# Optimization experiments

Hardware: AMD Instinct MI355X
Metric: run time of the kernel (lower is better)

The kernel has to match this reference:

```python
import jax, jax.numpy as jnp
import numpy as np

B = 128        # graphs
N_PER = 1024   # nodes per graph
K = 7          # knn neighbors
X_SIZE = 16
POS_SIZE = 3
H1, H2 = 64, 128
N = B * N_PER
EPS = 1e-5


def _lin_init(key, din, dout):
    kw, kb = jax.random.split(key)
    s = 1.0 / np.sqrt(din)
    w = jax.random.uniform(kw, (din, dout), jnp.float32, -s, s)
    b = jax.random.uniform(kb, (dout,), jnp.float32, -s, s)
    return w, b


def setup_inputs() -> dict:
    key = jax.random.key(0)
    ks = jax.random.split(key, 12)
    x = jax.random.normal(ks[0], (N, X_SIZE), jnp.float32)
    pos = jax.random.normal(ks[1], (N, POS_SIZE), jnp.float32)
    batch = jnp.repeat(jnp.arange(B, dtype=jnp.int32), N_PER)
    wk1, bk1 = _lin_init(ks[2], X_SIZE, H1)
    wq1, bq1 = _lin_init(ks[3], X_SIZE, H1)
    wv1, bv1 = _lin_init(ks[4], X_SIZE, H1)
    ws1, bs1 = _lin_init(ks[5], X_SIZE, H1)
    wk2, bk2 = _lin_init(ks[6], H1, H2)
    wq2, bq2 = _lin_init(ks[7], H1, H2)
    wv2, bv2 = _lin_init(ks[8], H1, H2)
    ws2, bs2 = _lin_init(ks[9], H1, H2)
    g1 = jnp.ones((H1,), jnp.float32); be1 = jnp.zeros((H1,), jnp.float32)
    g2 = jnp.ones((H2,), jnp.float32); be2 = jnp.zeros((H2,), jnp.float32)
    return dict(x=x, pos=pos, batch=batch,
                wk1=wk1, bk1=bk1, wq1=wq1, bq1=bq1, wv1=wv1, bv1=bv1, ws1=ws1, bs1=bs1, g1=g1, be1=be1,
                wk2=wk2, bk2=bk2, wq2=wq2, bq2=bq2, wv2=wv2, bv2=bv2, ws2=ws2, bs2=bs2, g2=g2, be2=be2)


def knn_edges(pos):
    # batch-aware kNN: graphs are equal-sized contiguous blocks of N_PER nodes
    p = pos.reshape(B, N_PER, POS_SIZE)
    def per_graph(pg):
        d = jnp.sum((pg[:, None, :] - pg[None, :, :]) ** 2, axis=-1)  # [n, n]
        d = jnp.where(jnp.eye(N_PER, dtype=bool), jnp.inf, d)          # no self loops
        _, idx = jax.lax.top_k(-d, K)                                   # [n, K]
        return idx
    idx = jax.vmap(per_graph)(p)                       # [B, N_PER, K]
    offs = (jnp.arange(B) * N_PER)[:, None, None]
    src = (idx + offs).reshape(-1)                     # neighbor j (source)
    dst = jnp.broadcast_to(jnp.arange(N_PER)[None, :, None] + offs, (B, N_PER, K)).reshape(-1)
    return src, dst


def res_gated_conv(x, src, dst, wk, bk, wq, bq, wv, bv, ws, bs):
    # out_i = skip(x_i) + sum_{j->i} sigmoid(K x_i + Q x_j) * V x_j
    kf = x @ wk + bk
    qf = x @ wq + bq
    vf = x @ wv + bv
    msg = jax.nn.sigmoid(kf[dst] + qf[src]) * vf[src]  # [E, out]
    agg = jnp.zeros_like(kf).at[dst].add(msg)
    return agg + x @ ws + bs


def batch_norm(x, gamma, beta):
    m = x.mean(0)
    v = jnp.mean((x - m) ** 2, 0)  # biased var (training-mode BN)
    return (x - m) * jax.lax.rsqrt(v + EPS) * gamma + beta


def reference(x, pos, batch, wk1, bk1, wq1, bq1, wv1, bv1, ws1, bs1, g1, be1,
              wk2, bk2, wq2, bq2, wv2, bv2, ws2, bs2, g2, be2):
    src, dst = knn_edges(pos)
    h = jax.nn.relu(batch_norm(res_gated_conv(x, src, dst, wk1, bk1, wq1, bq1, wv1, bv1, ws1, bs1), g1, be1))
    h = jax.nn.relu(batch_norm(res_gated_conv(h, src, dst, wk2, bk2, wq2, bq2, wv2, bv2, ws2, bs2), g2, be2))
    s = jax.ops.segment_sum(h, batch, num_segments=B)
    cnt = jax.ops.segment_sum(jnp.ones((h.shape[0], 1), h.dtype), batch, num_segments=B)
    return s / cnt
```

## Files before the change

kernel.cpp:

```cpp
#include <hip/hip_runtime.h>
#include <hip/hip_bf16.h>

#define BGR   128
#define NPER  1024
#define NK    7
#define NNODES (BGR*NPER)

typedef __attribute__((ext_vector_type(8))) short short8;
typedef __attribute__((ext_vector_type(8))) unsigned short ushort8;
typedef __attribute__((ext_vector_type(4))) float floatx4;

static __device__ __forceinline__ float bf2f(unsigned short u) {
    unsigned int x = ((unsigned int)u) << 16;
    return __builtin_bit_cast(float, x);
}
static __device__ __forceinline__ unsigned short f2bf(float f) {
    unsigned int x = __builtin_bit_cast(unsigned int, f);
    unsigned int lsb = (x >> 16) & 1u;
    x += 0x7fffu + lsb;
    return (unsigned short)(x >> 16);
}

__global__ __launch_bounds__(256) void knn_kernel(const float* __restrict__ pos,
                                                  int* __restrict__ idx) {
    __shared__ __align__(16) floatx4 sp[NPER];
    __shared__ float ex[256][9];
    int g     = blockIdx.x >> 3;
    int qbase = (blockIdx.x & 7) << 7;
    int base  = g * NPER;
    const float* pg = pos + (size_t)base * 3;
    for (int t = threadIdx.x; t < NPER * 3; t += 256) {
        float v = pg[t];
        int j = t / 3, comp = t - j * 3;
        ((float*)&sp[j])[comp] = v;
    }
    __syncthreads();
    for (int j = threadIdx.x; j < NPER; j += 256) {
        floatx4 q = sp[j];
        sp[j].w = fmaf(q.x, q.x, fmaf(q.y, q.y, q.z * q.z));
    }
    __syncthreads();

    int qi = qbase + (threadIdx.x & 127);
    int hf = threadIdx.x >> 7;
    floatx4 me = sp[qi];
    float m2x = -2.f * me.x, m2y = -2.f * me.y, m2z = -2.f * me.z;

    float b0=3e38f,b1=3e38f,b2=3e38f,b3=3e38f,b4=3e38f,b5=3e38f,b6=3e38f,b7=3e38f;
    int j0base = hf << 9;
    for (int j0 = j0base; j0 < j0base + 512; j0 += 8) {
        #pragma unroll
        for (int u = 0; u < 8; ++u) {
            floatx4 q = sp[j0 + u];
            float d = fmaf(m2x, q.x, fmaf(m2y, q.y, fmaf(m2z, q.z, q.w)));
            unsigned int ub = (__builtin_bit_cast(unsigned int, d) & 0xFFFFFC00u)
                              | (unsigned int)(j0 + u);
            float t = __builtin_bit_cast(float, ub);
            float n7 = __builtin_amdgcn_fmed3f(b6, b7, t);
            float n6 = __builtin_amdgcn_fmed3f(b5, b6, t);
            float n5 = __builtin_amdgcn_fmed3f(b4, b5, t);
            float n4 = __builtin_amdgcn_fmed3f(b3, b4, t);
            float n3 = __builtin_amdgcn_fmed3f(b2, b3, t);
            float n2 = __builtin_amdgcn_fmed3f(b1, b2, t);
            float n1 = __builtin_amdgcn_fmed3f(b0, b1, t);
            b0 = fminf(b0, t);
            b1 = n1; b2 = n2; b3 = n3; b4 = n4; b5 = n5; b6 = n6; b7 = n7;
        }
    }
    float* er = ex[threadIdx.x];
    er[0]=b0; er[1]=b1; er[2]=b2; er[3]=b3; er[4]=b4; er[5]=b5; er[6]=b6; er[7]=b7;
    __syncthreads();
    if (threadIdx.x < 128) {
        int sh = qi >> 9;
        const float* A  = ex[threadIdx.x + (sh << 7)];
        const float* Bo = ex[threadIdx.x + ((1 - sh) << 7)];
        int* op = idx + (size_t)(base + qi) * NK;
        #pragma unroll
        for (int i = 0; i < 7; ++i) {
            float mm = fminf(A[i + 1], Bo[6 - i]);
            op[i] = base + (int)(__builtin_bit_cast(unsigned int, mm) & 1023u);
        }
    }
}

__global__ __launch_bounds__(256) void feat1_kernel(
    const float* __restrict__ x,
    const float* __restrict__ wk, const float* __restrict__ bk,
    const float* __restrict__ wq, const float* __restrict__ bq,
    const float* __restrict__ wv, const float* __restrict__ bv,
    const float* __restrict__ wsm, const float* __restrict__ bs,
    unsigned int* __restrict__ qv, unsigned int* __restrict__ ks) {
    int c = threadIdx.x & 63;
    float Wk[16], Wq[16], Wv[16], Ws[16];
    #pragma unroll
    for (int k = 0; k < 16; ++k) {
        Wk[k] = wk[k*64+c]; Wq[k] = wq[k*64+c]; Wv[k] = wv[k*64+c]; Ws[k] = wsm[k*64+c];
    }
    float Bk = bk[c], Bq = bq[c], Bv = bv[c], Bs = bs[c];
    int wave = blockIdx.x * (blockDim.x >> 6) + (threadIdx.x >> 6);
    int nw   = gridDim.x * (blockDim.x >> 6);
    for (int n = wave; n < NNODES; n += nw) {
        const float* xr = x + (size_t)n * 16;
        float ak = Bk, aq = Bq, av = Bv, as = Bs;
        #pragma unroll
        for (int k = 0; k < 16; ++k) {
            float xv = xr[k];
            ak += xv * Wk[k]; aq += xv * Wq[k]; av += xv * Wv[k]; as += xv * Ws[k];
        }
        size_t o = (size_t)n * 64 + c;
        qv[o] = ((unsigned int)f2bf(av) << 16) | f2bf(aq);
        ks[o] = ((unsigned int)f2bf(as) << 16) | f2bf(ak);
    }
}

template<int C>
__global__ __launch_bounds__(256) void conv_kernel(
    const unsigned int* __restrict__ qv, const unsigned int* __restrict__ ks,
    const int* __restrict__ idx, unsigned short* __restrict__ h,
    float* __restrict__ part) {
    const int NPB = 256 / C;
    int c   = threadIdx.x & (C - 1);
    int sub = __builtin_amdgcn_readfirstlane((int)(threadIdx.x / C));
    int b     = blockIdx.x;
    int xcd   = b & 7;
    int chunk = b >> 3;
    int graph = xcd * 16 + (chunk >> 5);
    int nblk  = chunk & 31;
    int n0 = graph * NPER + nblk * 32;
    float s = 0.f, s2 = 0.f;
    #pragma unroll 2
    for (int i = sub; i < 32; i += NPB) {
        int n = n0 + i;
        const int* nb = idx + (size_t)n * NK;
        unsigned int ku = ks[(size_t)n * C + c];
        float kv  = bf2f((unsigned short)(ku & 0xFFFF));
        float acc = bf2f((unsigned short)(ku >> 16));
        #pragma unroll
        for (int k = 0; k < NK; ++k) {
            int j = __builtin_amdgcn_readfirstlane(nb[k]);
            const unsigned int* p = qv + (size_t)j * C;
            unsigned int u = p[c];
            float qvv = bf2f((unsigned short)(u & 0xFFFF));
            float vvv = bf2f((unsigned short)(u >> 16));
            float t = kv + qvv;
            float sg = __builtin_amdgcn_rcpf(1.f + __expf(-t));
            acc = fmaf(sg, vvv, acc);
        }
        unsigned short hb = f2bf(acc);
        h[(size_t)n * C + c] = hb;
        float hv = bf2f(hb);
        s += hv; s2 += hv * hv;
    }
    __shared__ float ls[256], ls2[256];
    ls[threadIdx.x] = s; ls2[threadIdx.x] = s2;
    __syncthreads();
    if (threadIdx.x < C) {
        #pragma unroll
        for (int l = 1; l < NPB; ++l) { s += ls[threadIdx.x + l*C]; s2 += ls2[threadIdx.x + l*C]; }
        part[(size_t)blockIdx.x * 2 * C + threadIdx.x]     = s;
        part[(size_t)blockIdx.x * 2 * C + C + threadIdx.x] = s2;
    }
}

template<int C>
static __device__ __forceinline__ void bnfin_body(
    const float* __restrict__ part, const float* __restrict__ gamma,
    const float* __restrict__ beta, float* __restrict__ ss,
    int c, float* ls, float* ls2) {
    float s = 0.f, s2 = 0.f;
    for (int b = threadIdx.x; b < 4096; b += 256) {
        s  += part[(size_t)b * 2 * C + c];
        s2 += part[(size_t)b * 2 * C + C + c];
    }
    ls[threadIdx.x] = s; ls2[threadIdx.x] = s2;
    __syncthreads();
    for (int st = 128; st > 0; st >>= 1) {
        if (threadIdx.x < st) { ls[threadIdx.x] += ls[threadIdx.x+st]; ls2[threadIdx.x] += ls2[threadIdx.x+st]; }
        __syncthreads();
    }
    if (threadIdx.x == 0) {
        float m   = ls[0] / (float)NNODES;
        float var = ls2[0] / (float)NNODES - m * m;
        float inv = rsqrtf(var + 1e-5f);
        float sc  = gamma[c] * inv;
        ss[c]     = sc;
        ss[C + c] = beta[c] - m * sc;
    }
}

template<int C>
__global__ __launch_bounds__(256) void bnfin_kernel(
    const float* __restrict__ part, const float* __restrict__ gamma,
    const float* __restrict__ beta, float* __restrict__ ss) {
    __shared__ float ls[256], ls2[256];
    bnfin_body<C>(part, gamma, beta, ss, blockIdx.x, ls, ls2);
}

__global__ __launch_bounds__(256) void fin1_wfrag_kernel(
    const float* __restrict__ part, const float* __restrict__ gamma,
    const float* __restrict__ beta, float* __restrict__ ss,
    const float* __restrict__ w0, const float* __restrict__ w1,
    const float* __restrict__ w2, const float* __restrict__ w3,
    unsigned short* __restrict__ frag) {
    __shared__ float ls[256], ls2[256];
    if (blockIdx.x < 64) {
        bnfin_body<64>(part, gamma, beta, ss, blockIdx.x, ls, ls2);
        return;
    }
    int s  = blockIdx.x - 64;
    if (threadIdx.x >= 64) return;
    int m  = s >> 4;
    int kt = (s >> 3) & 1;
    int ct = s & 7;
    const float* w = (m == 0) ? w0 : (m == 1) ? w1 : (m == 2) ? w2 : w3;
    int l = threadIdx.x;
    int col = ct * 16 + (l & 15);
    int kbase = kt * 32 + (l >> 4) * 8;
    unsigned short* out = frag + ((size_t)s * 64 + l) * 8;
    #pragma unroll
    for (int e = 0; e < 8; ++e) out[e] = f2bf(w[(size_t)(kbase + e) * 128 + col]);
}

__global__ __launch_bounds__(256) void feat2_kernel(
    const unsigned short* __restrict__ h1n, const unsigned short* __restrict__ frag,
    const float* __restrict__ ss1,
    const float* __restrict__ b0, const float* __restrict__ b1,
    const float* __restrict__ b2, const float* __restrict__ b3,
    unsigned int* __restrict__ qv2, unsigned int* __restrict__ ks2) {
    __shared__ unsigned short xh[2][2][16][17];
    int nt = blockIdx.x;
    int m  = threadIdx.x >> 6;
    int l  = threadIdx.x & 63;
    const float* bm = (m == 0) ? b0 : (m == 1) ? b1 : (m == 2) ? b2 : b3;
    int lr = l & 15;
    int gq = l >> 4;
    int n  = nt * 16 + lr;
    const unsigned short* ar = h1n + (size_t)n * 64 + gq * 8;
    short8 a0r = *(const short8*)ar;
    short8 a1r = *(const short8*)(ar + 32);
    short8 a0, a1;
    #pragma unroll
    for (int e = 0; e < 8; ++e) {
        int c0 = gq * 8 + e;
        float f0 = bf2f((unsigned short)a0r[e]) * ss1[c0] + ss1[64 + c0];
        a0[e] = (short)f2bf(fmaxf(f0, 0.f));
        int c1 = 32 + gq * 8 + e;
        float f1 = bf2f((unsigned short)a1r[e]) * ss1[c1] + ss1[64 + c1];
        a1[e] = (short)f2bf(fmaxf(f1, 0.f));
    }
    #pragma unroll
    for (int ct = 0; ct < 8; ++ct) {
        size_t fb0 = ((size_t)(m * 16 + ct)     * 64 + l) * 8;
        size_t fb1 = ((size_t)(m * 16 + 8 + ct) * 64 + l) * 8;
        short8 w0 = *(const short8*)(frag + fb0);
        short8 w1 = *(const short8*)(frag + fb1);
        float bv = bm[ct * 16 + lr];
        floatx4 acc = {bv, bv, bv, bv};
        acc = __builtin_amdgcn_mfma_f32_16x16x32_bf16(a0, w0, acc, 0, 0, 0);
        acc = __builtin_amdgcn_mfma_f32_16x16x32_bf16(a1, w1, acc, 0, 0, 0);
        if (m >= 2) {
            #pragma unroll
            for (int r = 0; r < 4; ++r)
                xh[ct & 1][m - 2][gq * 4 + r][lr] = f2bf(acc[r]);
        }
        __syncthreads();
        if (m < 2) {
            unsigned int* od = (m == 1) ? qv2 : ks2;
            int set = (m == 1) ? 0 : 1;
            #pragma unroll
            for (int r = 0; r < 4; ++r) {
                unsigned int lo = f2bf(acc[r]);
                unsigned int hi = xh[ct & 1][set][gq * 4 + r][lr];
                od[(size_t)(nt * 16 + gq * 4 + r) * 128 + ct * 16 + lr] = (hi << 16) | lo;
            }
        }
    }
}

__global__ __launch_bounds__(256) void pool_partial_kernel(const unsigned short* __restrict__ h2,
                                                           const float* __restrict__ ss2,
                                                           float* __restrict__ part) {
    int g = blockIdx.x >> 2;
    int q = blockIdx.x & 3;
    int c = threadIdx.x & 127;
    int isub = threadIdx.x >> 7;
    float sc = ss2[c], sh = ss2[128 + c];
    float acc = 0.f;
    const unsigned short* hp = h2 + ((size_t)g * NPER + q * 256) * 128;
    for (int i = isub; i < 256; i += 2)
        acc += fmaxf(bf2f(hp[(size_t)i * 128 + c]) * sc + sh, 0.f);
    __shared__ float red[256];
    red[threadIdx.x] = acc;
    __syncthreads();
    if (threadIdx.x < 128)
        part[(size_t)blockIdx.x * 128 + c] = acc + red[threadIdx.x + 128];
}

__global__ void pool_final_kernel(const float* __restrict__ part, float* __restrict__ out) {
    int g = blockIdx.x, c = threadIdx.x;
    float s = part[(size_t)(g*4+0)*128+c] + part[(size_t)(g*4+1)*128+c]
            + part[(size_t)(g*4+2)*128+c] + part[(size_t)(g*4+3)*128+c];
    out[(size_t)g * 128 + c] = s * (1.f / 1024.f);
}

extern "C" void kernel_launch(void* const* d_in, const int* in_sizes, int n_in,
                              void* d_out, int out_size, void* d_ws, size_t ws_size,
                              hipStream_t stream) {
    const float* x   = (const float*)d_in[0];
    const float* pos = (const float*)d_in[1];
    const float* wk1 = (const float*)d_in[3];
    const float* bk1 = (const float*)d_in[4];
    const float* wq1 = (const float*)d_in[5];
    const float* bq1 = (const float*)d_in[6];
    const float* wv1 = (const float*)d_in[7];
    const float* bv1 = (const float*)d_in[8];
    const float* ws1 = (const float*)d_in[9];
    const float* bs1 = (const float*)d_in[10];
    const float* g1  = (const float*)d_in[11];
    const float* be1 = (const float*)d_in[12];
    const float* wk2 = (const float*)d_in[13];
    const float* bk2 = (const float*)d_in[14];
    const float* wq2 = (const float*)d_in[15];
    const float* bq2 = (const float*)d_in[16];
    const float* wv2 = (const float*)d_in[17];
    const float* bv2 = (const float*)d_in[18];
    const float* ws2 = (const float*)d_in[19];
    const float* bs2 = (const float*)d_in[20];
    const float* g2  = (const float*)d_in[21];
    const float* be2 = (const float*)d_in[22];
    float* out = (float*)d_out;

    const size_t SZ_QV1 = (size_t)NNODES * 64 * 4;
    const size_t SZ_QV2 = (size_t)NNODES * 128 * 4;

    char* ws = (char*)d_ws;
    size_t off = 0;
    auto alloc = [&](size_t b) { size_t o = off; off += (b + 255) & ~(size_t)255; return o; };

    int* idx              = (int*)(ws + alloc((size_t)NNODES * NK * 4));
    size_t o_region       = alloc(2 * SZ_QV2);
    unsigned int* qv1     = (unsigned int*)(ws + o_region);
    unsigned int* ks1     = (unsigned int*)(ws + o_region + SZ_QV1);
    unsigned int* qv2     = (unsigned int*)(ws + o_region);
    unsigned int* ks2     = (unsigned int*)(ws + o_region + SZ_QV2);
    unsigned short* h1    = (unsigned short*)(ws + alloc((size_t)NNODES * 64 * 2));
    unsigned short* h2    = (unsigned short*)(ws + alloc((size_t)NNODES * 128 * 2));
    unsigned short* frag  = (unsigned short*)(ws + alloc(64 * 64 * 8 * 2));
    float* part           = (float*)(ws + alloc((size_t)4096 * 2 * 128 * 4));
    float* ss1            = (float*)(ws + alloc(2 * 64 * 4));
    float* ss2            = (float*)(ws + alloc(2 * 128 * 4));
    (void)ws_size; (void)in_sizes; (void)n_in; (void)out_size;

    knn_kernel<<<BGR * 8, 256, 0, stream>>>(pos, idx);
    feat1_kernel<<<1024, 256, 0, stream>>>(x, wk1, bk1, wq1, bq1, wv1, bv1, ws1, bs1,
                                           qv1, ks1);
    conv_kernel<64><<<NNODES / 32, 256, 0, stream>>>(qv1, ks1, idx, h1, part);
    fin1_wfrag_kernel<<<128, 256, 0, stream>>>(part, g1, be1, ss1,
                                               wk2, wq2, wv2, ws2, frag);
    feat2_kernel<<<NNODES / 16, 256, 0, stream>>>(h1, frag, ss1, bk2, bq2, bv2, bs2,
                                                  qv2, ks2);
    conv_kernel<128><<<NNODES / 32, 256, 0, stream>>>(qv2, ks2, idx, h2, part);
    bnfin_kernel<128><<<128, 256, 0, stream>>>(part, g2, be2, ss2);
    pool_partial_kernel<<<BGR * 4, 256, 0, stream>>>(h2, ss2, part);
    pool_final_kernel<<<BGR, 128, 0, stream>>>(part, out);
}
```

Baseline: 257.3 us.

## Precompute padded positions globally and read kNN candidates via uniform scalar loads

Adds a small prep kernel that writes each position as a float4 with its squared norm in the w lane. The kNN kernel drops its shared-memory staging and two barriers and instead loads candidate points straight from global memory. Because the half index is made wave-uniform with readfirstlane, those loads can become scalar loads. This removes LDS traffic and the sync overhead from the inner loop, at the cost of one extra kernel launch and relying on scalar-cache hits.

```diff
diff --git a/kernel.cpp b/kernel.cpp
--- a/kernel.cpp
+++ b/kernel.cpp
@@ -21,37 +21,39 @@
     return (unsigned short)(x >> 16);
 }
 
-__global__ __launch_bounds__(256) void knn_kernel(const float* __restrict__ pos,
+__global__ __launch_bounds__(256) void prep_pos_kernel(const float* __restrict__ pos,
+                                                       floatx4* __restrict__ p4) {
+    int i = blockIdx.x * 256 + threadIdx.x;
+    if (i < NNODES) {
+        float x = pos[(size_t)i*3], y = pos[(size_t)i*3+1], z = pos[(size_t)i*3+2];
+        floatx4 v;
+        v.x = x; v.y = y; v.z = z;
+        v.w = fmaf(x, x, fmaf(y, y, z * z));
+        p4[i] = v;
+    }
+}
+
+__global__ __launch_bounds__(256) void knn_kernel(const floatx4* __restrict__ p4,
                                                   int* __restrict__ idx) {
-    __shared__ __align__(16) floatx4 sp[NPER];
     __shared__ float ex[256][9];
     int g     = blockIdx.x >> 3;
     int qbase = (blockIdx.x & 7) << 7;
     int base  = g * NPER;
-    const float* pg = pos + (size_t)base * 3;
-    for (int t = threadIdx.x; t < NPER * 3; t += 256) {
-        float v = pg[t];
-        int j = t / 3, comp = t - j * 3;
-        ((float*)&sp[j])[comp] = v;
-    }
-    __syncthreads();
-    for (int j = threadIdx.x; j < NPER; j += 256) {
-        floatx4 q = sp[j];
-        sp[j].w = fmaf(q.x, q.x, fmaf(q.y, q.y, q.z * q.z));
-    }
-    __syncthreads();
-
     int qi = qbase + (threadIdx.x & 127);
-    int hf = threadIdx.x >> 7;
-    floatx4 me = sp[qi];
+    int hf = __builtin_amdgcn_readfirstlane((int)(threadIdx.x >> 7));
+    floatx4 me = p4[base + qi];
     float m2x = -2.f * me.x, m2y = -2.f * me.y, m2z = -2.f * me.z;
+    const floatx4* cp = p4 + base;
 
     float b0=3e38f,b1=3e38f,b2=3e38f,b3=3e38f,b4=3e38f,b5=3e38f,b6=3e38f,b7=3e38f;
     int j0base = hf << 9;
     for (int j0 = j0base; j0 < j0base + 512; j0 += 8) {
+        floatx4 qq[8];
+        #pragma unroll
+        for (int u = 0; u < 8; ++u) qq[u] = cp[j0 + u];
         #pragma unroll
         for (int u = 0; u < 8; ++u) {
-            floatx4 q = sp[j0 + u];
+            floatx4 q = qq[u];
             float d = fmaf(m2x, q.x, fmaf(m2y, q.y, fmaf(m2z, q.z, q.w)));
             unsigned int ub = (__builtin_bit_cast(unsigned int, d) & 0xFFFFFC00u)
                               | (unsigned int)(j0 + u);
@@ -349,9 +351,11 @@
     float* part           = (float*)(ws + alloc((size_t)4096 * 2 * 128 * 4));
     float* ss1            = (float*)(ws + alloc(2 * 64 * 4));
     float* ss2            = (float*)(ws + alloc(2 * 128 * 4));
+    floatx4* p4           = (floatx4*)(ws + alloc((size_t)NNODES * 16));
     (void)ws_size; (void)in_sizes; (void)n_in; (void)out_size;
 
-    knn_kernel<<<BGR * 8, 256, 0, stream>>>(pos, idx);
+    prep_pos_kernel<<<NNODES / 256, 256, 0, stream>>>(pos, p4);
+    knn_kernel<<<BGR * 8, 256, 0, stream>>>(p4, idx);
     feat1_kernel<<<1024, 256, 0, stream>>>(x, wk1, bk1, wq1, bq1, wv1, bv1, ws1, bs1,
                                            qv1, ks1);
     conv_kernel<64><<<NNODES / 32, 256, 0, stream>>>(qv1, ks1, idx, h1, part);
```

After: 267.3 us. 3.9% more time.
